# Kernel optimization log

Measured on AMD Instinct MI355X. Metric: run time of the kernel, lower is better.

The kernel has to match this reference:

```python
import jax, jax.numpy as jnp
import numpy as np

EPS = 1e-5

def _lc(x, w, b, stride, pad):
    # x: [B,H,W]; w: [Ho,Wo,kh,kw]; b: [Ho,Wo]
    Ho, Wo, kh, kw = w.shape
    patches = jax.lax.conv_general_dilated_patches(
        x[:, None], (kh, kw), (stride, stride), [(pad, pad), (pad, pad)])
    # patches: [B, kh*kw, Ho, Wo]
    out = jnp.einsum('bkij,ijk->bij', patches, w.reshape(Ho, Wo, kh * kw))
    return out + b

def _ln2d(x, g, b):
    # torch LayerNorm over the last two (spatial) dims
    mu = x.mean(axis=(1, 2), keepdims=True)
    var = ((x - mu) ** 2).mean(axis=(1, 2), keepdims=True)
    return (x - mu) * jax.lax.rsqrt(var + EPS) * g + b

def _pool(x):
    # MaxPool2d(kernel=2, stride=2) over spatial dims of [B,H,W]
    return jax.lax.reduce_window(x, -jnp.inf, jax.lax.max, (1, 2, 2), (1, 2, 2), 'VALID')

def setup_inputs() -> dict:
    key = jax.random.key(0)
    ks = jax.random.split(key, 32)
    d = {}
    d['x'] = jax.random.normal(ks[0], (64, 128, 128), jnp.float32)
    sizes = [(128, 7), (64, 5), (64, 5), (32, 3), (32, 3), (16, 3)]
    for i, (s, k) in enumerate(sizes, start=1):
        d[f'w{i}'] = jax.random.normal(ks[4 * i], (s, s, k, k), jnp.float32) / k
        d[f'b{i}'] = jax.random.normal(ks[4 * i + 1], (s, s), jnp.float32)
        d[f'g{i}'] = jnp.ones((s, s), jnp.float32)
        d[f'be{i}'] = jnp.zeros((s, s), jnp.float32)
    d['fcw'] = jax.random.normal(ks[30], (1024, 256), jnp.float32) / np.sqrt(256.0)
    d['fcb'] = jax.random.normal(ks[31], (1024,), jnp.float32) * 0.01
    return d

def reference(x, w1, b1, g1, be1, w2, b2, g2, be2, w3, b3, g3, be3,
              w4, b4, g4, be4, w5, b5, g5, be5, w6, b6, g6, be6, fcw, fcb):
    # dropout is identity (eval / p=0)
    h = _pool(_ln2d(jax.nn.relu(_lc(x, w1, b1, 1, 3)), g1, be1))   # [B,64,64]
    h = _ln2d(jax.nn.relu(_lc(h, w2, b2, 1, 2)), g2, be2)          # [B,64,64]
    h = _pool(_ln2d(jax.nn.relu(_lc(h, w3, b3, 1, 2)), g3, be3))   # [B,32,32]
    h = _ln2d(jax.nn.relu(_lc(h, w4, b4, 1, 1)), g4, be4)          # [B,32,32]
    h = _pool(_ln2d(jax.nn.relu(_lc(h, w5, b5, 1, 1)), g5, be5))   # [B,16,16]
    h = _ln2d(jax.nn.relu(_lc(h, w6, b6, 1, 1)), g6, be6)          # [B,16,16]
    h = h.reshape(h.shape[0], -1) @ fcw.T + fcb                    # [B,1024]
    return jax.nn.softmax(h, axis=-1)
```

## Files before the change

kernel.cpp:

```cpp
#include <hip/hip_runtime.h>

#define LN_EPS 1e-5f

constexpr int T1_OFF   = 0;
constexpr int WT2_OFF  = 1048576;
constexpr int WT3_OFF  = WT2_OFF + 102400;
constexpr int WT4_OFF  = WT3_OFF + 102400;
constexpr int WT5_OFF  = WT4_OFF + 9216;
constexpr int WT6_OFF  = WT5_OFF + 9216;
constexpr int FCWT_OFF = WT6_OFF + 2304;

constexpr int NREP = 136;

__global__ __launch_bounds__(256) void s1_conv(const float* __restrict__ x,
                                               const float* __restrict__ w1,
                                               const float* __restrict__ b1,
                                               const float* __restrict__ w2,
                                               const float* __restrict__ w3,
                                               const float* __restrict__ w4,
                                               const float* __restrict__ w5,
                                               const float* __restrict__ w6,
                                               const float* __restrict__ fcw,
                                               float* __restrict__ ws)
{
    const int tid = threadIdx.x;

    if (blockIdx.x < NREP) {
        const int rb = blockIdx.x;
        if (rb < 32) {
            for (int idx = rb * 256 + tid; idx < 102400; idx += 32 * 256) {
                int p = idx / 25, k = idx % 25;
                ws[WT2_OFF + k * 4096 + p] = w2[idx];
            }
        } else if (rb < 64) {
            for (int idx = (rb - 32) * 256 + tid; idx < 102400; idx += 32 * 256) {
                int p = idx / 25, k = idx % 25;
                ws[WT3_OFF + k * 4096 + p] = w3[idx];
            }
        } else if (rb < 68) {
            for (int idx = (rb - 64) * 256 + tid; idx < 9216; idx += 4 * 256) {
                int p = idx / 9, k = idx % 9;
                ws[WT4_OFF + k * 1024 + p] = w4[idx];
            }
        } else if (rb < 72) {
            for (int idx = (rb - 68) * 256 + tid; idx < 9216; idx += 4 * 256) {
                int p = idx / 9, k = idx % 9;
                ws[WT5_OFF + k * 1024 + p] = w5[idx];
            }
        } else if (rb < 73) {
            for (int idx = tid; idx < 2304; idx += 256) {
                int p = idx / 9, k = idx % 9;
                ws[WT6_OFF + k * 256 + p] = w6[idx];
            }
        } else {
            for (int idx = (rb - 73) * 256 + tid; idx < 262144; idx += 63 * 256) {
                int r = idx >> 8, k = idx & 255;
                ws[FCWT_OFF + k * 1024 + r] = fcw[idx];
            }
        }
        return;
    }

    constexpr int R = 128, K = 7, TILE = 8, S = 16, PAD = 3;
    constexpr int RT = TILE + K - 1;
    constexpr int PP = RT * RT + 1;
    constexpr int NBLK = R / TILE;
    constexpr int WCNT = TILE * TILE * K * K;
    constexpr int PG = 256 / S;
    constexpr int OPT = TILE * TILE / PG;

    __shared__ float s_in[S * PP];
    __shared__ float s_w[WCNT];
    __shared__ float s_b[TILE * TILE];

    float* t1 = ws + T1_OFF;
    const int cb = blockIdx.x - NREP;
    const int bt = cb % (NBLK * NBLK);
    const int sg = cb / (NBLK * NBLK);
    const int i0 = (bt / NBLK) * TILE;
    const int j0 = (bt % NBLK) * TILE;
    const int S0 = sg * S;

    for (int idx = tid; idx < WCNT; idx += 256) {
        int pi = idx / (K * K), kk = idx % (K * K);
        int gi = i0 + pi / TILE, gj = j0 + pi % TILE;
        s_w[idx] = w1[(gi * R + gj) * (K * K) + kk];
    }
    if (tid < TILE * TILE)
        s_b[tid] = b1[(i0 + tid / TILE) * R + (j0 + tid % TILE)];

    for (int idx = tid; idx < S * RT * RT; idx += 256) {
        int ls = idx / (RT * RT), p = idx % (RT * RT);
        int ci = i0 - PAD + p / RT, cj = j0 - PAD + p % RT;
        float v = 0.0f;
        if (ci >= 0 && ci < R && cj >= 0 && cj < R)
            v = x[(S0 + ls) * R * R + ci * R + cj];
        s_in[ls * PP + p] = v;
    }
    __syncthreads();

    const int s = tid % S;
    const int pg = tid / S;
    const int p0 = pg * OPT;
    const int ti = p0 / TILE, tj0 = p0 % TILE;
    float acc[OPT];
    #pragma unroll
    for (int o = 0; o < OPT; o++) acc[o] = s_b[p0 + o];
    #pragma unroll
    for (int ki = 0; ki < K; ki++) {
        float row[OPT + K - 1];
        #pragma unroll
        for (int c = 0; c < OPT + K - 1; c++)
            row[c] = s_in[s * PP + (ti + ki) * RT + tj0 + c];
        #pragma unroll
        for (int kj = 0; kj < K; kj++)
            #pragma unroll
            for (int o = 0; o < OPT; o++)
                acc[o] += row[o + kj] * s_w[(p0 + o) * (K * K) + ki * K + kj];
    }
    #pragma unroll
    for (int o = 0; o < OPT; o++)
        t1[(S0 + s) * R * R + (i0 + ti) * R + (j0 + tj0 + o)] = fmaxf(acc[o], 0.0f);
}

constexpr int NT = 1024;
constexpr int NW = NT / 64;

__device__ __forceinline__ void stats_reduce(float* red, float lsum, float lsq,
                                             float inv_n, float* s_mu, float* s_rs)
{
    const int tid = threadIdx.x;
    #pragma unroll
    for (int off = 32; off > 0; off >>= 1) {
        lsum += __shfl_down(lsum, off, 64);
        lsq  += __shfl_down(lsq,  off, 64);
    }
    if ((tid & 63) == 0) { red[tid >> 6] = lsum; red[NW + (tid >> 6)] = lsq; }
    __syncthreads();
    if (tid == 0) {
        float a = 0.f, b = 0.f;
        #pragma unroll
        for (int i = 0; i < NW; i++) { a += red[i]; b += red[NW + i]; }
        float mu = a * inv_n, ms = b * inv_n;
        *s_mu = mu;
        *s_rs = rsqrtf(ms - mu * mu + LN_EPS);
    }
    __syncthreads();
}

template<int M, int K>
__device__ __forceinline__ void conv_t(const float* __restrict__ I,
                                       const float* __restrict__ wT,
                                       const float* __restrict__ bias,
                                       float* __restrict__ R,
                                       float& lsum, float& lsq)
{
    constexpr int NPOS = M * M;
    constexpr int PADK = (K - 1) / 2;
    constexpr int STR = M + 1;
    constexpr int OPT = (NPOS + NT - 1) / NT;
    const int tid = threadIdx.x;

    #pragma unroll
    for (int o = 0; o < OPT; o++) {
        int p = tid + o * NT;
        if (NPOS < NT && p >= NPOS) break;
        int i = p / M, j = p % M;
        float acc = bias[p];
        #pragma unroll
        for (int ki = 0; ki < K; ki++) {
            int ii = i - PADK + ki;
            bool rok = (ii >= 0 && ii < M);
            #pragma unroll
            for (int kj = 0; kj < K; kj++) {
                int jj = j - PADK + kj;
                float iv = (rok && jj >= 0 && jj < M) ? I[ii * STR + jj] : 0.0f;
                acc += iv * wT[(ki * K + kj) * NPOS + p];
            }
        }
        float v = fmaxf(acc, 0.0f);
        R[i * STR + j] = v;
        lsum += v;
        lsq  += v * v;
    }
}

template<int N, bool POOL>
__device__ __forceinline__ void transform(const float* __restrict__ R,
                                          float mu, float rs,
                                          const float* __restrict__ g,
                                          const float* __restrict__ b,
                                          float* __restrict__ I)
{
    constexpr int M = POOL ? N / 2 : N;
    constexpr int SR = N + 1, SI = M + 1;
    const int tid = threadIdx.x;
    for (int p = tid; p < M * M; p += NT) {
        int i = p / M, j = p % M;
        float v;
        if constexpr (POOL) {
            float best = -3.4e38f;
            #pragma unroll
            for (int dy = 0; dy < 2; dy++)
                #pragma unroll
                for (int dx = 0; dx < 2; dx++) {
                    int r = 2 * i + dy, c = 2 * j + dx;
                    float n = (R[r * SR + c] - mu) * rs * g[r * N + c] + b[r * N + c];
                    best = fmaxf(best, n);
                }
            v = best;
        } else {
            v = (R[i * SR + j] - mu) * rs * g[i * N + j] + b[i * N + j];
        }
        I[i * SI + j] = v;
    }
}

__global__ __launch_bounds__(1024) void tail_fused(
    const float* __restrict__ ws_ro,
    const float* __restrict__ g1, const float* __restrict__ be1,
    const float* __restrict__ b2,
    const float* __restrict__ g2, const float* __restrict__ be2,
    const float* __restrict__ b3,
    const float* __restrict__ g3, const float* __restrict__ be3,
    const float* __restrict__ b4,
    const float* __restrict__ g4, const float* __restrict__ be4,
    const float* __restrict__ b5,
    const float* __restrict__ g5, const float* __restrict__ be5,
    const float* __restrict__ b6,
    const float* __restrict__ g6, const float* __restrict__ be6,
    const float* __restrict__ fcb,
    float* __restrict__ outp)
{
    __shared__ __align__(16) float I[64 * 65];
    __shared__ __align__(16) float R[64 * 65];
    __shared__ __align__(16) float h[256];
    __shared__ float red[2 * NW];
    __shared__ float s_mu, s_rs;

    const int s = blockIdx.x;
    const int tid = threadIdx.x;
    const float* x1 = ws_ro + T1_OFF + s * 16384;
    const float* wT2 = ws_ro + WT2_OFF;
    const float* wT3 = ws_ro + WT3_OFF;
    const float* wT4 = ws_ro + WT4_OFF;
    const float* wT5 = ws_ro + WT5_OFF;
    const float* wT6 = ws_ro + WT6_OFF;
    const float* fcwT = ws_ro + FCWT_OFF;

    float ls = 0.f, lq = 0.f;
    const float4* x4 = (const float4*)x1;
    #pragma unroll
    for (int i = tid; i < 4096; i += NT) {
        float4 v = x4[i];
        ls += v.x + v.y + v.z + v.w;
        lq += v.x * v.x + v.y * v.y + v.z * v.z + v.w * v.w;
    }
    stats_reduce(red, ls, lq, 1.f / 16384.f, &s_mu, &s_rs);

    {
        float mu = s_mu, rs = s_rs;
        for (int p = tid; p < 4096; p += NT) {
            int i = p >> 6, j = p & 63;
            float best = -3.4e38f;
            #pragma unroll
            for (int dy = 0; dy < 2; dy++)
                #pragma unroll
                for (int dx = 0; dx < 2; dx++) {
                    int r = 2 * i + dy, c = 2 * j + dx;
                    float n = (x1[r * 128 + c] - mu) * rs * g1[r * 128 + c] + be1[r * 128 + c];
                    best = fmaxf(best, n);
                }
            I[i * 65 + j] = best;
        }
    }
    __syncthreads();

    ls = lq = 0.f; conv_t<64, 5>(I, wT2, b2, R, ls, lq);
    stats_reduce(red, ls, lq, 1.f / 4096.f, &s_mu, &s_rs);
    transform<64, false>(R, s_mu, s_rs, g2, be2, I);
    __syncthreads();

    ls = lq = 0.f; conv_t<64, 5>(I, wT3, b3, R, ls, lq);
    stats_reduce(red, ls, lq, 1.f / 4096.f, &s_mu, &s_rs);
    transform<64, true>(R, s_mu, s_rs, g3, be3, I);
    __syncthreads();

    ls = lq = 0.f; conv_t<32, 3>(I, wT4, b4, R, ls, lq);
    stats_reduce(red, ls, lq, 1.f / 1024.f, &s_mu, &s_rs);
    transform<32, false>(R, s_mu, s_rs, g4, be4, I);
    __syncthreads();

    ls = lq = 0.f; conv_t<32, 3>(I, wT5, b5, R, ls, lq);
    stats_reduce(red, ls, lq, 1.f / 1024.f, &s_mu, &s_rs);
    transform<32, true>(R, s_mu, s_rs, g5, be5, I);
    __syncthreads();

    ls = lq = 0.f; conv_t<16, 3>(I, wT6, b6, R, ls, lq);
    stats_reduce(red, ls, lq, 1.f / 256.f, &s_mu, &s_rs);

    if (tid < 256) {
        int i = tid >> 4, j = tid & 15;
        h[tid] = (R[i * 17 + j] - s_mu) * s_rs * g6[tid] + be6[tid];
    }
    __syncthreads();

    float acc = fcb[tid];
    #pragma unroll 8
    for (int k = 0; k < 256; k++)
        acc += fcwT[k * 1024 + tid] * h[k];

    float m = acc;
    #pragma unroll
    for (int off = 32; off > 0; off >>= 1)
        m = fmaxf(m, __shfl_down(m, off, 64));
    if ((tid & 63) == 0) red[tid >> 6] = m;
    __syncthreads();
    if (tid == 0) {
        float mm = red[0];
        #pragma unroll
        for (int i = 1; i < NW; i++) mm = fmaxf(mm, red[i]);
        s_mu = mm;
    }
    __syncthreads();
    float e = expf(acc - s_mu);
    float sum = e;
    #pragma unroll
    for (int off = 32; off > 0; off >>= 1)
        sum += __shfl_down(sum, off, 64);
    if ((tid & 63) == 0) red[NW + (tid >> 6)] = sum;
    __syncthreads();
    if (tid == 0) {
        float ss = 0.f;
        #pragma unroll
        for (int i = 0; i < NW; i++) ss += red[NW + i];
        s_rs = 1.0f / ss;
    }
    __syncthreads();
    outp[s * 1024 + tid] = e * s_rs;
}

extern "C" void kernel_launch(void* const* d_in, const int* in_sizes, int n_in,
                              void* d_out, int out_size, void* d_ws, size_t ws_size,
                              hipStream_t stream) {
    (void)in_sizes; (void)n_in; (void)out_size; (void)ws_size;

    const float* x   = (const float*)d_in[0];
    const float* w1  = (const float*)d_in[1];  const float* b1  = (const float*)d_in[2];
    const float* g1  = (const float*)d_in[3];  const float* be1 = (const float*)d_in[4];
    const float* w2  = (const float*)d_in[5];  const float* b2  = (const float*)d_in[6];
    const float* g2  = (const float*)d_in[7];  const float* be2 = (const float*)d_in[8];
    const float* w3  = (const float*)d_in[9];  const float* b3  = (const float*)d_in[10];
    const float* g3  = (const float*)d_in[11]; const float* be3 = (const float*)d_in[12];
    const float* w4  = (const float*)d_in[13]; const float* b4  = (const float*)d_in[14];
    const float* g4  = (const float*)d_in[15]; const float* be4 = (const float*)d_in[16];
    const float* w5  = (const float*)d_in[17]; const float* b5  = (const float*)d_in[18];
    const float* g5  = (const float*)d_in[19]; const float* be5 = (const float*)d_in[20];
    const float* w6  = (const float*)d_in[21]; const float* b6  = (const float*)d_in[22];
    const float* g6  = (const float*)d_in[23]; const float* be6 = (const float*)d_in[24];
    const float* fcw = (const float*)d_in[25]; const float* fcb = (const float*)d_in[26];

    float* ws = (float*)d_ws;

    s1_conv<<<NREP + 1024, 256, 0, stream>>>(x, w1, b1, w2, w3, w4, w5, w6, fcw, ws);
    tail_fused<<<64, 1024, 0, stream>>>((const float*)ws,
        g1, be1, b2, g2, be2, b3, g3, be3,
        b4, g4, be4, b5, g5, be5, b6, g6, be6,
        fcb, (float*)d_out);
}
```

Baseline: 160.2 us.

## Vectorize tail stages with per-layer specialized conv, float4 loads and repacked FC weights

Replaces the generic templated conv and transform helpers with size-specialized versions. The 64x64 5x5 conv computes four adjacent outputs per thread from a shared register row window and float4 weight loads. The LDS row stride becomes padded to multiples of 4 so float4/float2 accesses are aligned, and the first pool-normalize stage uses vectorized global loads. FC weights are repacked into 4-wide k chunks so the final matvec uses float4 loads. The aim is fewer LDS and global load instructions and better register reuse, at the cost that the padded strides may raise LDS bank conflicts.

```diff
diff --git a/kernel.cpp b/kernel.cpp
--- a/kernel.cpp
+++ b/kernel.cpp
@@ -54,8 +54,9 @@
             }
         } else {
             for (int idx = (rb - 73) * 256 + tid; idx < 262144; idx += 63 * 256) {
-                int r = idx >> 8, k = idx & 255;
-                ws[FCWT_OFF + k * 1024 + r] = fcw[idx];
+                int r = idx >> 8, kc = idx & 255;
+                int kq = kc >> 2, c = kc & 3;
+                ws[FCWT_OFF + kq * 4096 + r * 4 + c] = fcw[idx];
             }
         }
         return;
@@ -148,72 +149,162 @@
     __syncthreads();
 }
 
-template<int M, int K>
-__device__ __forceinline__ void conv_t(const float* __restrict__ I,
-                                       const float* __restrict__ wT,
-                                       const float* __restrict__ bias,
-                                       float* __restrict__ R,
-                                       float& lsum, float& lsq)
-{
-    constexpr int NPOS = M * M;
-    constexpr int PADK = (K - 1) / 2;
-    constexpr int STR = M + 1;
-    constexpr int OPT = (NPOS + NT - 1) / NT;
-    const int tid = threadIdx.x;
-
-    #pragma unroll
-    for (int o = 0; o < OPT; o++) {
-        int p = tid + o * NT;
-        if (NPOS < NT && p >= NPOS) break;
-        int i = p / M, j = p % M;
-        float acc = bias[p];
-        #pragma unroll
-        for (int ki = 0; ki < K; ki++) {
-            int ii = i - PADK + ki;
-            bool rok = (ii >= 0 && ii < M);
-            #pragma unroll
-            for (int kj = 0; kj < K; kj++) {
-                int jj = j - PADK + kj;
-                float iv = (rok && jj >= 0 && jj < M) ? I[ii * STR + jj] : 0.0f;
-                acc += iv * wT[(ki * K + kj) * NPOS + p];
-            }
-        }
-        float v = fmaxf(acc, 0.0f);
-        R[i * STR + j] = v;
-        lsum += v;
-        lsq  += v * v;
-    }
-}
-
-template<int N, bool POOL>
-__device__ __forceinline__ void transform(const float* __restrict__ R,
-                                          float mu, float rs,
-                                          const float* __restrict__ g,
-                                          const float* __restrict__ b,
-                                          float* __restrict__ I)
-{
-    constexpr int M = POOL ? N / 2 : N;
-    constexpr int SR = N + 1, SI = M + 1;
-    const int tid = threadIdx.x;
-    for (int p = tid; p < M * M; p += NT) {
-        int i = p / M, j = p % M;
-        float v;
-        if constexpr (POOL) {
-            float best = -3.4e38f;
-            #pragma unroll
-            for (int dy = 0; dy < 2; dy++)
-                #pragma unroll
-                for (int dx = 0; dx < 2; dx++) {
-                    int r = 2 * i + dy, c = 2 * j + dx;
-                    float n = (R[r * SR + c] - mu) * rs * g[r * N + c] + b[r * N + c];
-                    best = fmaxf(best, n);
-                }
-            v = best;
-        } else {
-            v = (R[i * SR + j] - mu) * rs * g[i * N + j] + b[i * N + j];
-        }
-        I[i * SI + j] = v;
-    }
+__device__ __forceinline__ void conv64_5(const float* __restrict__ I,
+                                         const float* __restrict__ wT,
+                                         const float* __restrict__ bias,
+                                         float* __restrict__ R,
+                                         float& lsum, float& lsq)
+{
+    const int tid = threadIdx.x;
+    const int i  = tid >> 4;
+    const int j0 = (tid & 15) << 2;
+    float4 bv = ((const float4*)bias)[tid];
+    float a0 = bv.x, a1 = bv.y, a2 = bv.z, a3 = bv.w;
+    #pragma unroll
+    for (int ki = 0; ki < 5; ki++) {
+        int ii = i - 2 + ki;
+        bool rok = (ii >= 0 && ii < 64);
+        float row[8];
+        #pragma unroll
+        for (int c = 0; c < 8; c++) {
+            int jj = j0 - 2 + c;
+            row[c] = (rok && jj >= 0 && jj < 64) ? I[ii * 68 + jj] : 0.f;
+        }
+        #pragma unroll
+        for (int kj = 0; kj < 5; kj++) {
+            float4 wv = ((const float4*)(wT + (ki * 5 + kj) * 4096))[tid];
+            a0 += row[kj + 0] * wv.x;
+            a1 += row[kj + 1] * wv.y;
+            a2 += row[kj + 2] * wv.z;
+            a3 += row[kj + 3] * wv.w;
+        }
+    }
+    float4 o;
+    o.x = fmaxf(a0, 0.f); o.y = fmaxf(a1, 0.f);
+    o.z = fmaxf(a2, 0.f); o.w = fmaxf(a3, 0.f);
+    *((float4*)(R + i * 68 + j0)) = o;
+    lsum += o.x + o.y + o.z + o.w;
+    lsq  += o.x * o.x + o.y * o.y + o.z * o.z + o.w * o.w;
+}
+
+__device__ __forceinline__ void conv32_3(const float* __restrict__ I,
+                                         const float* __restrict__ wT,
+                                         const float* __restrict__ bias,
+                                         float* __restrict__ R,
+                                         float& lsum, float& lsq)
+{
+    const int tid = threadIdx.x;
+    const int i = tid >> 5, j = tid & 31;
+    float acc = bias[tid];
+    #pragma unroll
+    for (int ki = 0; ki < 3; ki++) {
+        int ii = i - 1 + ki;
+        bool rok = (ii >= 0 && ii < 32);
+        float r0 = (rok && j >= 1)  ? I[ii * 36 + j - 1] : 0.f;
+        float r1 = rok              ? I[ii * 36 + j]     : 0.f;
+        float r2 = (rok && j <= 30) ? I[ii * 36 + j + 1] : 0.f;
+        acc += r0 * wT[(ki * 3 + 0) * 1024 + tid]
+             + r1 * wT[(ki * 3 + 1) * 1024 + tid]
+             + r2 * wT[(ki * 3 + 2) * 1024 + tid];
+    }
+    float v = fmaxf(acc, 0.f);
+    R[i * 36 + j] = v;
+    lsum += v; lsq += v * v;
+}
+
+__device__ __forceinline__ void conv16_3(const float* __restrict__ I,
+                                         const float* __restrict__ wT,
+                                         const float* __restrict__ bias,
+                                         float* __restrict__ R,
+                                         float& lsum, float& lsq)
+{
+    const int tid = threadIdx.x;
+    if (tid >= 256) return;
+    const int i = tid >> 4, j = tid & 15;
+    float acc = bias[tid];
+    #pragma unroll
+    for (int ki = 0; ki < 3; ki++) {
+        int ii = i - 1 + ki;
+        bool rok = (ii >= 0 && ii < 16);
+        float r0 = (rok && j >= 1)  ? I[ii * 20 + j - 1] : 0.f;
+        float r1 = rok              ? I[ii * 20 + j]     : 0.f;
+        float r2 = (rok && j <= 14) ? I[ii * 20 + j + 1] : 0.f;
+        acc += r0 * wT[(ki * 3 + 0) * 256 + tid]
+             + r1 * wT[(ki * 3 + 1) * 256 + tid]
+             + r2 * wT[(ki * 3 + 2) * 256 + tid];
+    }
+    float v = fmaxf(acc, 0.f);
+    R[i * 20 + j] = v;
+    lsum += v; lsq += v * v;
+}
+
+__device__ __forceinline__ void t64(const float* __restrict__ R, float mu, float rs,
+                                    const float* __restrict__ g,
+                                    const float* __restrict__ b,
+                                    float* __restrict__ I)
+{
+    const int tid = threadIdx.x;
+    const int i = tid >> 4, j0 = (tid & 15) << 2;
+    float4 rv = *((const float4*)(R + i * 68 + j0));
+    float4 gv = ((const float4*)g)[tid];
+    float4 bv = ((const float4*)b)[tid];
+    float4 o;
+    o.x = (rv.x - mu) * rs * gv.x + bv.x;
+    o.y = (rv.y - mu) * rs * gv.y + bv.y;
+    o.z = (rv.z - mu) * rs * gv.z + bv.z;
+    o.w = (rv.w - mu) * rs * gv.w + bv.w;
+    *((float4*)(I + i * 68 + j0)) = o;
+}
+
+__device__ __forceinline__ void t64pool(const float* __restrict__ R, float mu, float rs,
+                                        const float* __restrict__ g,
+                                        const float* __restrict__ b,
+                                        float* __restrict__ I)
+{
+    const int tid = threadIdx.x;
+    const int i = tid >> 5, j = tid & 31;
+    float2 r0 = *((const float2*)(R + (2 * i) * 68 + 2 * j));
+    float2 r1 = *((const float2*)(R + (2 * i + 1) * 68 + 2 * j));
+    float2 g0 = *((const float2*)(g + (2 * i) * 64 + 2 * j));
+    float2 g1 = *((const float2*)(g + (2 * i + 1) * 64 + 2 * j));
+    float2 b0 = *((const float2*)(b + (2 * i) * 64 + 2 * j));
+    float2 b1 = *((const float2*)(b + (2 * i + 1) * 64 + 2 * j));
+    float n00 = (r0.x - mu) * rs * g0.x + b0.x;
+    float n01 = (r0.y - mu) * rs * g0.y + b0.y;
+    float n10 = (r1.x - mu) * rs * g1.x + b1.x;
+    float n11 = (r1.y - mu) * rs * g1.y + b1.y;
+    I[i * 36 + j] = fmaxf(fmaxf(n00, n01), fmaxf(n10, n11));
+}
+
+__device__ __forceinline__ void t32(const float* __restrict__ R, float mu, float rs,
+                                    const float* __restrict__ g,
+                                    const float* __restrict__ b,
+                                    float* __restrict__ I)
+{
+    const int tid = threadIdx.x;
+    const int i = tid >> 5, j = tid & 31;
+    I[i * 36 + j] = (R[i * 36 + j] - mu) * rs * g[tid] + b[tid];
+}
+
+__device__ __forceinline__ void t32pool(const float* __restrict__ R, float mu, float rs,
+                                        const float* __restrict__ g,
+                                        const float* __restrict__ b,
+                                        float* __restrict__ I)
+{
+    const int tid = threadIdx.x;
+    if (tid >= 256) return;
+    const int i = tid >> 4, j = tid & 15;
+    float2 r0 = *((const float2*)(R + (2 * i) * 36 + 2 * j));
+    float2 r1 = *((const float2*)(R + (2 * i + 1) * 36 + 2 * j));
+    float2 g0 = *((const float2*)(g + (2 * i) * 32 + 2 * j));
+    float2 g1 = *((const float2*)(g + (2 * i + 1) * 32 + 2 * j));
+    float2 b0 = *((const float2*)(b + (2 * i) * 32 + 2 * j));
+    float2 b1 = *((const float2*)(b + (2 * i + 1) * 32 + 2 * j));
+    float n00 = (r0.x - mu) * rs * g0.x + b0.x;
+    float n01 = (r0.y - mu) * rs * g0.y + b0.y;
+    float n10 = (r1.x - mu) * rs * g1.x + b1.x;
+    float n11 = (r1.y - mu) * rs * g1.y + b1.y;
+    I[i * 20 + j] = fmaxf(fmaxf(n00, n01), fmaxf(n10, n11));
 }
 
 __global__ __launch_bounds__(1024) void tail_fused(
@@ -232,83 +323,109 @@
     const float* __restrict__ fcb,
     float* __restrict__ outp)
 {
-    __shared__ __align__(16) float I[64 * 65];
-    __shared__ __align__(16) float R[64 * 65];
+    __shared__ __align__(16) float I[64 * 68];
+    __shared__ __align__(16) float R[64 * 68];
     __shared__ __align__(16) float h[256];
     __shared__ float red[2 * NW];
     __shared__ float s_mu, s_rs;
 
     const int s = blockIdx.x;
     const int tid = threadIdx.x;
-    const float* x1 = ws_ro + T1_OFF + s * 16384;
+    const float* x1  = ws_ro + T1_OFF + s * 16384;
     const float* wT2 = ws_ro + WT2_OFF;
     const float* wT3 = ws_ro + WT3_OFF;
     const float* wT4 = ws_ro + WT4_OFF;
     const float* wT5 = ws_ro + WT5_OFF;
     const float* wT6 = ws_ro + WT6_OFF;
-    const float* fcwT = ws_ro + FCWT_OFF;
+    const float* fcwT4 = ws_ro + FCWT_OFF;
 
     float ls = 0.f, lq = 0.f;
-    const float4* x4 = (const float4*)x1;
-    #pragma unroll
-    for (int i = tid; i < 4096; i += NT) {
-        float4 v = x4[i];
-        ls += v.x + v.y + v.z + v.w;
-        lq += v.x * v.x + v.y * v.y + v.z * v.z + v.w * v.w;
+    {
+        const float4* x4 = (const float4*)x1;
+        #pragma unroll
+        for (int i = tid; i < 4096; i += NT) {
+            float4 v = x4[i];
+            ls += v.x + v.y + v.z + v.w;
+            lq += v.x * v.x + v.y * v.y + v.z * v.z + v.w * v.w;
+        }
     }
     stats_reduce(red, ls, lq, 1.f / 16384.f, &s_mu, &s_rs);
 
     {
         float mu = s_mu, rs = s_rs;
-        for (int p = tid; p < 4096; p += NT) {
-            int i = p >> 6, j = p & 63;
-            float best = -3.4e38f;
-            #pragma unroll
-            for (int dy = 0; dy < 2; dy++)
-                #pragma unroll
-                for (int dx = 0; dx < 2; dx++) {
-                    int r = 2 * i + dy, c = 2 * j + dx;
-                    float n = (x1[r * 128 + c] - mu) * rs * g1[r * 128 + c] + be1[r * 128 + c];
-                    best = fmaxf(best, n);
-                }
-            I[i * 65 + j] = best;
-        }
-    }
-    __syncthreads();
-
-    ls = lq = 0.f; conv_t<64, 5>(I, wT2, b2, R, ls, lq);
+        const int i = tid >> 4, j0 = (tid & 15) << 2;
+        const float* xr0 = x1 + (2 * i) * 128 + 2 * j0;
+        const float* xr1 = xr0 + 128;
+        const float* gr0 = g1 + (2 * i) * 128 + 2 * j0;
+        const float* gr1 = gr0 + 128;
+        const float* br0 = be1 + (2 * i) * 128 + 2 * j0;
+        const float* br1 = br0 + 128;
+        float4 xa0 = ((const float4*)xr0)[0], xa1 = ((const float4*)xr0)[1];
+        float4 xb0 = ((const float4*)xr1)[0], xb1 = ((const float4*)xr1)[1];
+        float4 ga0 = ((const float4*)gr0)[0], ga1 = ((const float4*)gr0)[1];
+        float4 gb0 = ((const float4*)gr1)[0], gb1 = ((const float4*)gr1)[1];
+        float4 ba0 = ((const float4*)br0)[0], ba1 = ((const float4*)br0)[1];
+        float4 bb0 = ((const float4*)br1)[0], bb1 = ((const float4*)br1)[1];
+        float xa[8] = {xa0.x, xa0.y, xa0.z, xa0.w, xa1.x, xa1.y, xa1.z, xa1.w};
+        float xb[8] = {xb0.x, xb0.y, xb0.z, xb0.w, xb1.x, xb1.y, xb1.z, xb1.w};
+        float ga[8] = {ga0.x, ga0.y, ga0.z, ga0.w, ga1.x, ga1.y, ga1.z, ga1.w};
+        float gb[8] = {gb0.x, gb0.y, gb0.z, gb0.w, gb1.x, gb1.y, gb1.z, gb1.w};
+        float ba[8] = {ba0.x, ba0.y, ba0.z, ba0.w, ba1.x, ba1.y, ba1.z, ba1.w};
+        float bb[8] = {bb0.x, bb0.y, bb0.z, bb0.w, bb1.x, bb1.y, bb1.z, bb1.w};
+        float4 o;
+        float* op = (float*)&o;
+        #pragma unroll
+        for (int c = 0; c < 4; c++) {
+            float n0 = (xa[2 * c]     - mu) * rs * ga[2 * c]     + ba[2 * c];
+            float n1 = (xa[2 * c + 1] - mu) * rs * ga[2 * c + 1] + ba[2 * c + 1];
+            float n2 = (xb[2 * c]     - mu) * rs * gb[2 * c]     + bb[2 * c];
+            float n3 = (xb[2 * c + 1] - mu) * rs * gb[2 * c + 1] + bb[2 * c + 1];
+            op[c] = fmaxf(fmaxf(n0, n1), fmaxf(n2, n3));
+        }
+        *((float4*)(I + i * 68 + j0)) = o;
+    }
+    __syncthreads();
+
+    ls = lq = 0.f; conv64_5(I, wT2, b2, R, ls, lq);
     stats_reduce(red, ls, lq, 1.f / 4096.f, &s_mu, &s_rs);
-    transform<64, false>(R, s_mu, s_rs, g2, be2, I);
-    __syncthreads();
-
-    ls = lq = 0.f; conv_t<64, 5>(I, wT3, b3, R, ls, lq);
+    t64(R, s_mu, s_rs, g2, be2, I);
+    __syncthreads();
+
+    ls = lq = 0.f; conv64_5(I, wT3, b3, R, ls, lq);
     stats_reduce(red, ls, lq, 1.f / 4096.f, &s_mu, &s_rs);
-    transform<64, true>(R, s_mu, s_rs, g3, be3, I);
-    __syncthreads();
-
-    ls = lq = 0.f; conv_t<32, 3>(I, wT4, b4, R, ls, lq);
+    t64pool(R, s_mu, s_rs, g3, be3, I);
+    __syncthreads();
+
+    ls = lq = 0.f; conv32_3(I, wT4, b4, R, ls, lq);
     stats_reduce(red, ls, lq, 1.f / 1024.f, &s_mu, &s_rs);
-    transform<32, false>(R, s_mu, s_rs, g4, be4, I);
-    __syncthreads();
-
-    ls = lq = 0.f; conv_t<32, 3>(I, wT5, b5, R, ls, lq);
+    t32(R, s_mu, s_rs, g4, be4, I);
+    __syncthreads();
+
+    ls = lq = 0.f; conv32_3(I, wT5, b5, R, ls, lq);
     stats_reduce(red, ls, lq, 1.f / 1024.f, &s_mu, &s_rs);
-    transform<32, true>(R, s_mu, s_rs, g5, be5, I);
-    __syncthreads();
-
-    ls = lq = 0.f; conv_t<16, 3>(I, wT6, b6, R, ls, lq);
+    t32pool(R, s_mu, s_rs, g5, be5, I);
+    __syncthreads();
+
+    ls = lq = 0.f; conv16_3(I, wT6, b6, R, ls, lq);
     stats_reduce(red, ls, lq, 1.f / 256.f, &s_mu, &s_rs);
 
     if (tid < 256) {
         int i = tid >> 4, j = tid & 15;
-        h[tid] = (R[i * 17 + j] - s_mu) * s_rs * g6[tid] + be6[tid];
+        h[tid] = (R[i * 20 + j] - s_mu) * s_rs * g6[tid] + be6[tid];
     }
     __syncthreads();
 
     float acc = fcb[tid];
-    #pragma unroll 8
-    for (int k = 0; k < 256; k++)
-        acc += fcwT[k * 1024 + tid] * h[k];
+    {
+        const float4* wq = (const float4*)fcwT4;
+        const float4* h4 = (const float4*)h;
+        #pragma unroll 8
+        for (int kq = 0; kq < 64; kq++) {
+            float4 wv = wq[kq * 1024 + tid];
+            float4 hv = h4[kq];
+            acc += wv.x * hv.x + wv.y * hv.y + wv.z * hv.z + wv.w * hv.w;
+        }
+    }
 
     float m = acc;
     #pragma unroll
```

After: 163.3 us. No clear change (+1.9%).
